# Kernel optimization log

Measured on AMD Instinct MI355X. Metric: run time of the kernel, lower is better.

## Reference

```python
import jax, jax.numpy as jnp
import numpy as np

WS = 8        # window size
NH = 12       # num heads
EPS = 1e-5    # torch LayerNorm eps


def _rel_pos_index(ws):
    c = np.arange(ws)
    coords = np.stack(np.meshgrid(c, c, indexing='ij')).reshape(2, -1)  # [2, ws*ws]
    rel = coords[:, :, None] - coords[:, None, :]                        # [2, N, N]
    rel = rel.transpose(1, 2, 0).copy()
    rel[:, :, 0] += ws - 1
    rel[:, :, 1] += ws - 1
    rel[:, :, 0] *= 2 * ws - 1
    return jnp.asarray(rel.sum(-1))                                      # [N, N]

REL_IDX = _rel_pos_index(WS)


def _layernorm(x, g, b):
    mu = jnp.mean(x, axis=-1, keepdims=True)
    var = jnp.mean(jnp.square(x - mu), axis=-1, keepdims=True)
    return (x - mu) * jax.lax.rsqrt(var + EPS) * g + b


def setup_inputs() -> dict:
    key = jax.random.key(0)
    ks = jax.random.split(key, 16)
    B, L, C = 32, 4096, 384
    hid = 4 * C
    s = lambda fan_in: 1.0 / np.sqrt(fan_in)
    return {
        'x': jax.random.normal(ks[0], (B, L, C), jnp.float32),
        'norm1_g': jnp.ones((C,), jnp.float32),
        'norm1_b': jnp.zeros((C,), jnp.float32),
        'qkv_w': jax.random.normal(ks[1], (C, 3 * C), jnp.float32) * s(C),
        'qkv_b': jnp.zeros((3 * C,), jnp.float32),
        'proj_w': jax.random.normal(ks[2], (C, C), jnp.float32) * s(C),
        'proj_b': jnp.zeros((C,), jnp.float32),
        'rpb_table': jax.random.normal(ks[3], ((2 * WS - 1) ** 2, NH), jnp.float32) * 0.02,
        'norm2_g': jnp.ones((C,), jnp.float32),
        'norm2_b': jnp.zeros((C,), jnp.float32),
        'fc1_w': jax.random.normal(ks[4], (C, hid), jnp.float32) * s(C),
        'fc1_b': jnp.zeros((hid,), jnp.float32),
        'fc2_w': jax.random.normal(ks[5], (hid, C), jnp.float32) * s(hid),
        'fc2_b': jnp.zeros((C,), jnp.float32),
    }


def reference(x, norm1_g, norm1_b, qkv_w, qkv_b, proj_w, proj_b, rpb_table,
              norm2_g, norm2_b, fc1_w, fc1_b, fc2_w, fc2_b):
    B, L, C = x.shape
    H = W = int(L ** 0.5)
    N = WS * WS
    hd = C // NH
    scale = hd ** -0.5

    shortcut = x
    h = _layernorm(x, norm1_g, norm1_b)
    # window partition: (B,H,W,C) -> (B*nW, N, C)
    h = h.reshape(B, H // WS, WS, W // WS, WS, C)
    h = h.transpose(0, 1, 3, 2, 4, 5).reshape(-1, N, C)

    qkv = (h @ qkv_w + qkv_b).reshape(-1, N, 3, NH, hd).transpose(2, 0, 3, 1, 4)
    q, k, v = qkv[0] * scale, qkv[1], qkv[2]          # each [Bw, NH, N, hd]
    attn = jnp.einsum('bhnd,bhmd->bhnm', q, k)
    bias = rpb_table[REL_IDX.reshape(-1)].reshape(N, N, NH).transpose(2, 0, 1)
    attn = jax.nn.softmax(attn + bias[None], axis=-1)
    o = jnp.einsum('bhnm,bhmd->bhnd', attn, v)
    o = o.transpose(0, 2, 1, 3).reshape(-1, N, C)
    o = o @ proj_w + proj_b

    # window reverse: (B*nW, N, C) -> (B, L, C)
    o = o.reshape(B, H // WS, W // WS, WS, WS, C)
    o = o.transpose(0, 1, 3, 2, 4, 5).reshape(B, L, C)

    x = shortcut + o
    h2 = _layernorm(x, norm2_g, norm2_b)
    m = jax.nn.gelu(h2 @ fc1_w + fc1_b, approximate=False) @ fc2_w + fc2_b
    return x + m
```

## Files before the change

kernel.cpp:

```cpp
#include <hip/hip_runtime.h>

typedef __attribute__((ext_vector_type(4))) float f32x4;
typedef __attribute__((ext_vector_type(8))) short short8;
typedef unsigned short bfu16;

typedef const __attribute__((address_space(1))) void* as1cv;
typedef __attribute__((address_space(3))) void* as3v;
#define GLL16(gp, lp) __builtin_amdgcn_global_load_lds((as1cv)(const void*)(gp), (as3v)(void*)(lp), 16, 0, 0)

__device__ __forceinline__ bfu16 f2b(float f) {
    union { float f; unsigned u; } x; x.f = f;
    unsigned r = x.u + 0x7fffu + ((x.u >> 16) & 1u);
    return (bfu16)(r >> 16);
}

__global__ __launch_bounds__(256) void k_convw(const float* __restrict__ W, bfu16* __restrict__ Wt,
                                               int K, int N) {
    int idx = blockIdx.x * 256 + threadIdx.x;
    if (idx >= K * N) return;
    int k = idx / N, n = idx - k * N;
    Wt[(size_t)n * K + k] = f2b(W[idx]);
}

__global__ __launch_bounds__(256) void k_ln(const float* __restrict__ x, const float* __restrict__ g,
                                            const float* __restrict__ b, bfu16* __restrict__ y) {
    int wid = threadIdx.x >> 6, lane = threadIdx.x & 63;
    size_t row = (size_t)blockIdx.x * 4 + wid;
    const float* xr = x + row * 384;
    float v[6];
#pragma unroll
    for (int i = 0; i < 6; ++i) v[i] = xr[lane + i * 64];
    float s = 0.f;
#pragma unroll
    for (int i = 0; i < 6; ++i) s += v[i];
#pragma unroll
    for (int off = 1; off < 64; off <<= 1) s += __shfl_xor(s, off, 64);
    float mean = s * (1.0f / 384.0f);
    float q = 0.f;
#pragma unroll
    for (int i = 0; i < 6; ++i) { float d = v[i] - mean; q += d * d; }
#pragma unroll
    for (int off = 1; off < 64; off <<= 1) q += __shfl_xor(q, off, 64);
    float inv = rsqrtf(q * (1.0f / 384.0f) + 1e-5f);
    bfu16* yr = y + row * 384;
#pragma unroll
    for (int i = 0; i < 6; ++i) {
        int c = lane + i * 64;
        yr[c] = f2b((v[i] - mean) * inv * g[c] + b[c]);
    }
}

template <int EPI>
__global__ __launch_bounds__(256) void k_gemm(const bfu16* __restrict__ A, const bfu16* __restrict__ Bt,
                                              const float* __restrict__ bias, const float* __restrict__ res,
                                              float* __restrict__ outf, bfu16* __restrict__ outb,
                                              int N, int K) {
    __shared__ __align__(16) bfu16 As[128 * 32];
    __shared__ __align__(16) bfu16 Bs[128 * 32];
    const int tid = threadIdx.x, wid = tid >> 6, lane = tid & 63;
    const int quad = lane >> 4, l16 = lane & 15;
    const int m0 = blockIdx.y * 128, n0 = blockIdx.x * 128;
    const int wm = (wid >> 1) * 64, wn = (wid & 1) * 64;
    const bfu16* Ag = A + (size_t)(m0 + wid * 32 + (lane >> 2)) * K + (lane & 3) * 8;
    const bfu16* Bg = Bt + (size_t)(n0 + wid * 32 + (lane >> 2)) * K + (lane & 3) * 8;
    bfu16* Al0 = As + (wid * 32) * 32;
    bfu16* Al1 = As + (wid * 32 + 16) * 32;
    bfu16* Bl0 = Bs + (wid * 32) * 32;
    bfu16* Bl1 = Bs + (wid * 32 + 16) * 32;

    const f32x4 zero = {0.f, 0.f, 0.f, 0.f};
    f32x4 acc[4][4];
#pragma unroll
    for (int i = 0; i < 4; ++i)
#pragma unroll
        for (int j = 0; j < 4; ++j) acc[i][j] = zero;

    for (int k0 = 0; k0 < K; k0 += 32) {
        GLL16(Ag + k0, Al0);
        GLL16(Ag + k0 + 16 * K, Al1);
        GLL16(Bg + k0, Bl0);
        GLL16(Bg + k0 + 16 * K, Bl1);
        __syncthreads();
        short8 af[4], bfr[4];
#pragma unroll
        for (int t = 0; t < 4; ++t) af[t]  = *(const short8*)(As + (wm + t * 16 + l16) * 32 + quad * 8);
#pragma unroll
        for (int t = 0; t < 4; ++t) bfr[t] = *(const short8*)(Bs + (wn + t * 16 + l16) * 32 + quad * 8);
#pragma unroll
        for (int mt = 0; mt < 4; ++mt)
#pragma unroll
            for (int nt = 0; nt < 4; ++nt)
                acc[mt][nt] = __builtin_amdgcn_mfma_f32_16x16x32_bf16(af[mt], bfr[nt], acc[mt][nt], 0, 0, 0);
        __syncthreads();
    }

#pragma unroll
    for (int mt = 0; mt < 4; ++mt)
#pragma unroll
        for (int nt = 0; nt < 4; ++nt)
#pragma unroll
            for (int r = 0; r < 4; ++r) {
                int m = m0 + wm + mt * 16 + quad * 4 + r;
                int n = n0 + wn + nt * 16 + l16;
                float v = acc[mt][nt][r] + bias[n];
                size_t off = (size_t)m * N + n;
                if (EPI == 0) {
                    outb[off] = f2b(v);
                } else if (EPI == 1) {
                    outf[off] = v + res[off];
                } else {
                    float gv = 0.5f * v * (1.0f + erff(v * 0.70710678118654752f));
                    outb[off] = f2b(gv);
                }
            }
}

__global__ __launch_bounds__(256) void k_attn(const bfu16* __restrict__ qkv, const float* __restrict__ rpb,
                                              bfu16* __restrict__ o) {
    __shared__ __align__(16) bfu16 P_s[4][64 * 64];
    __shared__ __align__(16) bfu16 Vt_s[4][32 * 64];
    const int wid = threadIdx.x >> 6, lane = threadIdx.x & 63;
    const int quad = lane >> 4, l16 = lane & 15;
    const int gid = blockIdx.x * 4 + wid;
    const int win = gid / 12, head = gid - win * 12;
    const int b = win >> 6, wi = (win >> 3) & 7, wj = win & 7;
    const int rowbase = b * 4096 + wi * 8 * 64 + wj * 8;
#define ROWOF(t) (rowbase + ((t) >> 3) * 64 + ((t) & 7))

    {
        const bfu16* vr = qkv + (size_t)ROWOF(lane) * 1152 + 768 + head * 32;
        short8 v0 = *(const short8*)(vr);
        short8 v1 = *(const short8*)(vr + 8);
        short8 v2 = *(const short8*)(vr + 16);
        short8 v3 = *(const short8*)(vr + 24);
        bfu16* vt = &Vt_s[wid][0];
#pragma unroll
        for (int j = 0; j < 8; ++j) {
            vt[(0  + j) * 64 + lane] = (bfu16)v0[j];
            vt[(8  + j) * 64 + lane] = (bfu16)v1[j];
            vt[(16 + j) * 64 + lane] = (bfu16)v2[j];
            vt[(24 + j) * 64 + lane] = (bfu16)v3[j];
        }
    }

    short8 qf[4], kf[4];
#pragma unroll
    for (int t = 0; t < 4; ++t) {
        const size_t r = (size_t)ROWOF(t * 16 + l16) * 1152;
        qf[t] = *(const short8*)(qkv + r + head * 32 + quad * 8);
        kf[t] = *(const short8*)(qkv + r + 384 + head * 32 + quad * 8);
    }
    const f32x4 zero = {0.f, 0.f, 0.f, 0.f};
    f32x4 s[4][4];
#pragma unroll
    for (int ti = 0; ti < 4; ++ti)
#pragma unroll
        for (int tj = 0; tj < 4; ++tj)
            s[ti][tj] = __builtin_amdgcn_mfma_f32_16x16x32_bf16(qf[ti], kf[tj], zero, 0, 0, 0);

    const float scale = 0.17677669529663689f;
    float inv_l[4][4];
#pragma unroll
    for (int ti = 0; ti < 4; ++ti)
#pragma unroll
        for (int r = 0; r < 4; ++r) {
            int i = ti * 16 + quad * 4 + r;
            int yi = i >> 3, xi = i & 7;
            float mv = -1e30f;
#pragma unroll
            for (int tj = 0; tj < 4; ++tj) {
                int j = tj * 16 + l16;
                int idx = (yi - (j >> 3) + 7) * 15 + (xi - (j & 7) + 7);
                float sv = s[ti][tj][r] * scale + rpb[idx * 12 + head];
                s[ti][tj][r] = sv;
                mv = fmaxf(mv, sv);
            }
#pragma unroll
            for (int off = 1; off < 16; off <<= 1) mv = fmaxf(mv, __shfl_xor(mv, off, 64));
            float sum = 0.f;
#pragma unroll
            for (int tj = 0; tj < 4; ++tj) {
                float p = __expf(s[ti][tj][r] - mv);
                s[ti][tj][r] = p;
                sum += p;
            }
#pragma unroll
            for (int off = 1; off < 16; off <<= 1) sum += __shfl_xor(sum, off, 64);
            inv_l[ti][r] = 1.0f / sum;
        }

    bfu16* P = &P_s[wid][0];
#pragma unroll
    for (int ti = 0; ti < 4; ++ti)
#pragma unroll
        for (int tj = 0; tj < 4; ++tj)
#pragma unroll
            for (int r = 0; r < 4; ++r)
                P[(ti * 16 + quad * 4 + r) * 64 + tj * 16 + l16] = f2b(s[ti][tj][r]);
    __syncthreads();

    f32x4 oacc[4][2];
#pragma unroll
    for (int i = 0; i < 4; ++i) { oacc[i][0] = zero; oacc[i][1] = zero; }
#pragma unroll
    for (int ks = 0; ks < 2; ++ks) {
        short8 pa[4], vb[2];
#pragma unroll
        for (int mt = 0; mt < 4; ++mt) pa[mt] = *(const short8*)(P + (mt * 16 + l16) * 64 + ks * 32 + quad * 8);
#pragma unroll
        for (int nt = 0; nt < 2; ++nt) vb[nt] = *(const short8*)(&Vt_s[wid][(nt * 16 + l16) * 64 + ks * 32 + quad * 8]);
#pragma unroll
        for (int mt = 0; mt < 4; ++mt)
#pragma unroll
            for (int nt = 0; nt < 2; ++nt)
                oacc[mt][nt] = __builtin_amdgcn_mfma_f32_16x16x32_bf16(pa[mt], vb[nt], oacc[mt][nt], 0, 0, 0);
    }

#pragma unroll
    for (int mt = 0; mt < 4; ++mt)
#pragma unroll
        for (int nt = 0; nt < 2; ++nt)
#pragma unroll
            for (int r = 0; r < 4; ++r) {
                int i = mt * 16 + quad * 4 + r;
                int col = head * 32 + nt * 16 + l16;
                o[(size_t)ROWOF(i) * 384 + col] = f2b(oacc[mt][nt][r] * inv_l[mt][r]);
            }
#undef ROWOF
}

extern "C" void kernel_launch(void* const* d_in, const int* in_sizes, int n_in,
                              void* d_out, int out_size, void* d_ws, size_t ws_size,
                              hipStream_t stream) {
    const float* x      = (const float*)d_in[0];
    const float* n1g    = (const float*)d_in[1];
    const float* n1b    = (const float*)d_in[2];
    const float* qkv_w  = (const float*)d_in[3];
    const float* qkv_b  = (const float*)d_in[4];
    const float* proj_w = (const float*)d_in[5];
    const float* proj_b = (const float*)d_in[6];
    const float* rpb    = (const float*)d_in[7];
    const float* n2g    = (const float*)d_in[8];
    const float* n2b    = (const float*)d_in[9];
    const float* fc1_w  = (const float*)d_in[10];
    const float* fc1_b  = (const float*)d_in[11];
    const float* fc2_w  = (const float*)d_in[12];
    const float* fc2_b  = (const float*)d_in[13];
    float* out = (float*)d_out;

    char* ws = (char*)d_ws;
    size_t off = 0;
    auto alloc = [&](size_t bytes) { void* p = ws + off; off = (off + bytes + 255) & ~(size_t)255; return p; };
    bfu16* WqT = (bfu16*)alloc(442368ull * 2);
    bfu16* WpT = (bfu16*)alloc(147456ull * 2);
    bfu16* W1T = (bfu16*)alloc(589824ull * 2);
    bfu16* W2T = (bfu16*)alloc(589824ull * 2);
    bfu16* act = (bfu16*)alloc(50331648ull * 2);
    bfu16* big = (bfu16*)alloc(201326592ull * 2);
    float* x1  = (float*)alloc(50331648ull * 4);

    const int M = 131072;

    k_convw<<<dim3((442368 + 255) / 256), 256, 0, stream>>>(qkv_w, WqT, 384, 1152);
    k_convw<<<dim3((147456 + 255) / 256), 256, 0, stream>>>(proj_w, WpT, 384, 384);
    k_convw<<<dim3((589824 + 255) / 256), 256, 0, stream>>>(fc1_w, W1T, 384, 1536);
    k_convw<<<dim3((589824 + 255) / 256), 256, 0, stream>>>(fc2_w, W2T, 1536, 384);

    k_ln<<<dim3(M / 4), 256, 0, stream>>>(x, n1g, n1b, act);

    k_gemm<0><<<dim3(1152 / 128, M / 128), 256, 0, stream>>>(act, WqT, qkv_b, nullptr, nullptr, big, 1152, 384);

    k_attn<<<dim3(6144), 256, 0, stream>>>(big, rpb, act);

    k_gemm<1><<<dim3(384 / 128, M / 128), 256, 0, stream>>>(act, WpT, proj_b, x, x1, nullptr, 384, 384);

    k_ln<<<dim3(M / 4), 256, 0, stream>>>(x1, n2g, n2b, act);

    k_gemm<2><<<dim3(1536 / 128, M / 128), 256, 0, stream>>>(act, W1T, fc1_b, nullptr, nullptr, big, 1536, 384);

    k_gemm<1><<<dim3(384 / 128, M / 128), 256, 0, stream>>>(big, W2T, fc2_b, x1, out, nullptr, 384, 1536);
}
```

Before: 1.637 ms.

## Swizzle LDS layouts in GEMM and attention, use polynomial GELU, hoist bias loads

Applies XOR swizzles to the GEMM A/B shared tiles and to the attention P and V-transpose shared buffers to cut LDS bank conflicts. Replaces erff in the GELU epilogue with an Abramowitz-Stegun polynomial erf approximation using a hardware reciprocal and fast exp. Hoists the per-column bias loads out of the epilogue loop. The polynomial erf has about 1e-7 absolute error, below bf16 output rounding, and the swizzles must match exactly between writers and readers.

New measurement: 1.547 ms. -5.5%, faster.

```diff
diff --git a/kernel.cpp b/kernel.cpp
--- a/kernel.cpp
+++ b/kernel.cpp
@@ -13,6 +13,19 @@
     unsigned r = x.u + 0x7fffu + ((x.u >> 16) & 1u);
     return (bfu16)(r >> 16);
 }
+
+__device__ __forceinline__ float fast_gelu(float v) {
+    float z = v * 0.70710678118654752f;
+    float a = fabsf(z);
+    float t = __builtin_amdgcn_rcpf(fmaf(0.3275911f, a, 1.0f));
+    float poly = t * fmaf(t, fmaf(t, fmaf(t, fmaf(t, 1.061405429f, -1.453152027f), 1.421413741f), -0.284496736f), 0.254829592f);
+    float e = __expf(-a * a);
+    float erfa = fmaf(-poly, e, 1.0f);
+    float erfz = copysignf(erfa, z);
+    return 0.5f * v * (1.0f + erfz);
+}
+
+#define VSWZ(d) ((((d) ^ ((d) >> 3)) & 7))
 
 __global__ __launch_bounds__(256) void k_convw(const float* __restrict__ W, bfu16* __restrict__ Wt,
                                                int K, int N) {
@@ -61,12 +74,16 @@
     const int quad = lane >> 4, l16 = lane & 15;
     const int m0 = blockIdx.y * 128, n0 = blockIdx.x * 128;
     const int wm = (wid >> 1) * 64, wn = (wid & 1) * 64;
-    const bfu16* Ag = A + (size_t)(m0 + wid * 32 + (lane >> 2)) * K + (lane & 3) * 8;
-    const bfu16* Bg = Bt + (size_t)(n0 + wid * 32 + (lane >> 2)) * K + (lane & 3) * 8;
+    const int srow = lane >> 2;
+    const int skc = (lane & 3) ^ ((lane >> 3) & 3);
+    const bfu16* Ag = A + (size_t)(m0 + wid * 32 + srow) * K + skc * 8;
+    const bfu16* Bg = Bt + (size_t)(n0 + wid * 32 + srow) * K + skc * 8;
     bfu16* Al0 = As + (wid * 32) * 32;
     bfu16* Al1 = As + (wid * 32 + 16) * 32;
     bfu16* Bl0 = Bs + (wid * 32) * 32;
     bfu16* Bl1 = Bs + (wid * 32 + 16) * 32;
+
+    const int swq = (quad ^ ((l16 >> 1) & 3)) * 8;
 
     const f32x4 zero = {0.f, 0.f, 0.f, 0.f};
     f32x4 acc[4][4];
@@ -83,9 +100,9 @@
         __syncthreads();
         short8 af[4], bfr[4];
 #pragma unroll
-        for (int t = 0; t < 4; ++t) af[t]  = *(const short8*)(As + (wm + t * 16 + l16) * 32 + quad * 8);
-#pragma unroll
-        for (int t = 0; t < 4; ++t) bfr[t] = *(const short8*)(Bs + (wn + t * 16 + l16) * 32 + quad * 8);
+        for (int t = 0; t < 4; ++t) af[t]  = *(const short8*)(As + (wm + t * 16 + l16) * 32 + swq);
+#pragma unroll
+        for (int t = 0; t < 4; ++t) bfr[t] = *(const short8*)(Bs + (wn + t * 16 + l16) * 32 + swq);
 #pragma unroll
         for (int mt = 0; mt < 4; ++mt)
 #pragma unroll
@@ -94,6 +111,10 @@
         __syncthreads();
     }
 
+    float bv[4];
+#pragma unroll
+    for (int nt = 0; nt < 4; ++nt) bv[nt] = bias[n0 + wn + nt * 16 + l16];
+
 #pragma unroll
     for (int mt = 0; mt < 4; ++mt)
 #pragma unroll
@@ -102,15 +123,14 @@
             for (int r = 0; r < 4; ++r) {
                 int m = m0 + wm + mt * 16 + quad * 4 + r;
                 int n = n0 + wn + nt * 16 + l16;
-                float v = acc[mt][nt][r] + bias[n];
+                float v = acc[mt][nt][r] + bv[nt];
                 size_t off = (size_t)m * N + n;
                 if (EPI == 0) {
                     outb[off] = f2b(v);
                 } else if (EPI == 1) {
                     outf[off] = v + res[off];
                 } else {
-                    float gv = 0.5f * v * (1.0f + erff(v * 0.70710678118654752f));
-                    outb[off] = f2b(gv);
+                    outb[off] = f2b(fast_gelu(v));
                 }
             }
 }
@@ -134,12 +154,13 @@
         short8 v2 = *(const short8*)(vr + 16);
         short8 v3 = *(const short8*)(vr + 24);
         bfu16* vt = &Vt_s[wid][0];
+        const int lh = lane >> 3, ll = lane & 7;
 #pragma unroll
         for (int j = 0; j < 8; ++j) {
-            vt[(0  + j) * 64 + lane] = (bfu16)v0[j];
-            vt[(8  + j) * 64 + lane] = (bfu16)v1[j];
-            vt[(16 + j) * 64 + lane] = (bfu16)v2[j];
-            vt[(24 + j) * 64 + lane] = (bfu16)v3[j];
+            vt[(0  + j) * 64 + ((lh ^ VSWZ(0  + j)) * 8) + ll] = (bfu16)v0[j];
+            vt[(8  + j) * 64 + ((lh ^ VSWZ(8  + j)) * 8) + ll] = (bfu16)v1[j];
+            vt[(16 + j) * 64 + ((lh ^ VSWZ(16 + j)) * 8) + ll] = (bfu16)v2[j];
+            vt[(24 + j) * 64 + ((lh ^ VSWZ(24 + j)) * 8) + ll] = (bfu16)v3[j];
         }
     }
 
@@ -195,8 +216,11 @@
 #pragma unroll
         for (int tj = 0; tj < 4; ++tj)
 #pragma unroll
-            for (int r = 0; r < 4; ++r)
-                P[(ti * 16 + quad * 4 + r) * 64 + tj * 16 + l16] = f2b(s[ti][tj][r]);
+            for (int r = 0; r < 4; ++r) {
+                int i = ti * 16 + quad * 4 + r;
+                int j = tj * 16 + l16;
+                P[i * 64 + (((j >> 3) ^ VSWZ(i)) * 8) + (j & 7)] = f2b(s[ti][tj][r]);
+            }
     __syncthreads();
 
     f32x4 oacc[4][2];
@@ -206,9 +230,15 @@
     for (int ks = 0; ks < 2; ++ks) {
         short8 pa[4], vb[2];
 #pragma unroll
-        for (int mt = 0; mt < 4; ++mt) pa[mt] = *(const short8*)(P + (mt * 16 + l16) * 64 + ks * 32 + quad * 8);
-#pragma unroll
-        for (int nt = 0; nt < 2; ++nt) vb[nt] = *(const short8*)(&Vt_s[wid][(nt * 16 + l16) * 64 + ks * 32 + quad * 8]);
+        for (int mt = 0; mt < 4; ++mt) {
+            int rm = mt * 16 + l16;
+            pa[mt] = *(const short8*)(P + rm * 64 + (((ks * 4 + quad) ^ VSWZ(rm)) * 8));
+        }
+#pragma unroll
+        for (int nt = 0; nt < 2; ++nt) {
+            int rv = nt * 16 + l16;
+            vb[nt] = *(const short8*)(&Vt_s[wid][rv * 64 + (((ks * 4 + quad) ^ VSWZ(rv)) * 8)]);
+        }
 #pragma unroll
         for (int mt = 0; mt < 4; ++mt)
 #pragma unroll
```
